# Optimization experiments

Hardware: AMD Instinct MI355X
Metric: run time of the kernel (lower is better)

Reference implementation:

```python
import jax, jax.numpy as jnp
import numpy as np

B, N, C, H = 2, 2048, 256, 16
D = C // H  # head_dim = 16


def _res_linear(x, W, b):
    # ResidualMLP with num_layers=-1 and in_dim==out_dim, input/output residual: x + Linear(x)
    return x + x @ W.T + b


def _split_heads(z):
    # [B, N, H*D] -> [B, H, N, D]
    return z.reshape(B, N, H, D).transpose(0, 2, 1, 3)


def setup_inputs() -> dict:
    key = jax.random.key(0)
    ks = jax.random.split(key, 10)
    def lin(k):
        return 0.02 * jax.random.normal(k, (C, C), dtype=jnp.float32)
    inp = {
        'x': jax.random.normal(ks[0], (B, N, C), dtype=jnp.float32),
        'attention_mask': jnp.ones((B, N), dtype=jnp.float32),
        'Wq1': lin(ks[1]), 'bq1': jnp.zeros((C,), jnp.float32),
        'Wq2': lin(ks[2]), 'bq2': jnp.zeros((C,), jnp.float32),
        'Wq3': lin(ks[3]), 'bq3': jnp.zeros((C,), jnp.float32),
        'Wk1': lin(ks[4]), 'bk1': jnp.zeros((C,), jnp.float32),
        'Wk2': lin(ks[5]), 'bk2': jnp.zeros((C,), jnp.float32),
        'Wk3': lin(ks[6]), 'bk3': jnp.zeros((C,), jnp.float32),
        'Wv': lin(ks[7]), 'bv': jnp.zeros((C,), jnp.float32),
        'Wo': lin(ks[8]), 'bo': jnp.zeros((C,), jnp.float32),
        'gamma': jnp.ones((C,), jnp.float32),
        'beta': jnp.zeros((C,), jnp.float32),
    }
    return inp


def reference(x, attention_mask, Wq1, bq1, Wq2, bq2, Wq3, bq3,
              Wk1, bk1, Wk2, bk2, Wk3, bk3, Wv, bv, Wo, bo, gamma, beta):
    # residual single-linear projections (ResidualMLP num_layers=-1)
    q1 = _split_heads(_res_linear(x, Wq1, bq1))
    q2 = _split_heads(_res_linear(x, Wq2, bq2))
    q3 = _split_heads(_res_linear(x, Wq3, bq3))
    k1 = _split_heads(_res_linear(x, Wk1, bk1))
    k2 = _split_heads(_res_linear(x, Wk2, bk2))
    k3 = _split_heads(_res_linear(x, Wk3, bk3))
    v = _split_heads(_res_linear(x, Wv, bv))
    # kernel = identity; norm_q = norm_k = False
    mask = attention_mask[:, None, :, None]  # [B,1,N,1]
    q1, q2, q3 = q1 * mask, q2 * mask, q3 * mask
    k1, k2, k3, v = k1 * mask, k2 * mask, k3 * mask, v * mask
    scale = jnp.asarray(N, jnp.float32) ** -0.25
    k1, k2, k3, v = k1 * scale, k2 * scale, k3 * scale, v * scale
    # rank-4 state: [B,H,D,D,D,D]
    state = jnp.einsum('bhni,bhnj,bhnk,bhnl->bhijkl', k1, v, k2, k3, optimize=True)
    # contract queries with state: [B,H,N,D]
    out = jnp.einsum('bhni,bhijkl,bhnk,bhnl->bhnj', q1, state, q2, q3, optimize=True)
    out = out.transpose(0, 2, 1, 3).reshape(B, N, C)  # merge heads
    # LayerNorm(channel_dim), eps=1e-5
    mu = jnp.mean(out, axis=-1, keepdims=True)
    var = jnp.mean(jnp.square(out - mu), axis=-1, keepdims=True)
    out = (out - mu) * jax.lax.rsqrt(var + 1e-5) * gamma + beta
    out = out @ Wo.T + bo
    return out
```

## Files before the change

kernel.cpp:

```cpp
#include <hip/hip_runtime.h>
#include <hip/hip_bf16.h>


typedef _Float16 f16;
typedef _Float16 f16x8 __attribute__((ext_vector_type(8)));
typedef _Float16 f16x4 __attribute__((ext_vector_type(4)));
typedef float    f32x16 __attribute__((ext_vector_type(16)));
typedef uint32_t u32x4 __attribute__((ext_vector_type(4)));

#define MFMA32(a, b, c) __builtin_amdgcn_mfma_f32_32x32x16_f16((a), (b), (c), 0, 0, 0)

constexpr size_t OFF_XH  = 0;
constexpr size_t OFF_WH  = 2097152;
constexpr size_t OFF_BSC = 3014656;
constexpr size_t OFF_GH  = 3021824;
constexpr size_t OFF_RSG = 3152896;
constexpr size_t OFF_B2  = 3153920;
constexpr size_t OFF_Y   = 3154944;
constexpr size_t OFF_KH  = 9446400;
constexpr size_t OFF_VT  = 15737856;
constexpr size_t OFF_OPP = 17835008;

struct W7 { const float* W[7]; const float* b[7]; };

__device__ __forceinline__ int toff(int row, int oct) {
    return row * 128 + (((oct) ^ (row & 7)) << 4);
}
__device__ __forceinline__ f16x8 ldfrag(const f16* base, int row, int oct) {
    return *(const f16x8*)((const char*)base + toff(row, oct));
}
__device__ __forceinline__ void stfrag(f16* base, int row, int oct, f16x8 v) {
    *(f16x8*)((char*)base + toff(row, oct)) = v;
}
__device__ __forceinline__ int drow(int reg, int l) {
    return (reg & 3) + ((reg >> 2) << 3) + ((l >> 5) << 2);
}
__device__ __forceinline__ void zero16(f32x16& v) {
#pragma unroll
    for (int i = 0; i < 16; ++i) v[i] = 0.f;
}
__device__ __forceinline__ uint32_t pkrtz(float a, float b) {
    auto h = __builtin_amdgcn_cvt_pkrtz(a, b);
    return __builtin_bit_cast(uint32_t, h);
}

__global__ __launch_bounds__(256) void k_prep(const float* __restrict__ x, W7 p,
                                              float scale,
                                              const float* __restrict__ Wo,
                                              const float* __restrict__ bo,
                                              const float* __restrict__ gamma,
                                              const float* __restrict__ beta,
                                              char* ws) {
    const int bid = blockIdx.x;
    if (bid < 2824) {
        f16* xh  = (f16*)(ws + OFF_XH);
        f16* Wh  = (f16*)(ws + OFF_WH);
        float* bsc = (float*)(ws + OFF_BSC);
        int idx = bid * 256 + threadIdx.x;
        if (idx < 262144) {
            float4 v = ((const float4*)x)[idx];
            f16x4 o; o[0] = (f16)v.x; o[1] = (f16)v.y; o[2] = (f16)v.z; o[3] = (f16)v.w;
            *(f16x4*)(xh + (size_t)idx * 4) = o;
        } else if (idx < 262144 + 458752) {
            int r = idx - 262144;
            int t = r >> 16, cc = r & 65535, c = cc >> 8, k = cc & 255;
            float v = p.W[t][cc] + (c == k ? 1.f : 0.f);
            if (t >= 3) v *= scale;
            Wh[r] = (f16)v;
        } else if (idx < 262144 + 458752 + 1792) {
            int r = idx - 262144 - 458752;
            int t = r >> 8;
            bsc[r] = p.b[t][r & 255] * (t >= 3 ? scale : 1.f);
        }
    } else {
        f16* Gh = (f16*)(ws + OFF_GH);
        float* rsg = (float*)(ws + OFF_RSG);
        float* B2  = (float*)(ws + OFF_B2);
        int c2 = bid - 2824, c = threadIdx.x;
        float wv = Wo[c2 * 256 + c];
        float g = gamma[c] * wv;
        float bb = beta[c] * wv;
        Gh[c2 * 256 + c] = (f16)g;
        __shared__ float sg[4], sb[4];
#pragma unroll
        for (int off = 32; off > 0; off >>= 1) { g += __shfl_down(g, off); bb += __shfl_down(bb, off); }
        if ((c & 63) == 0) { sg[c >> 6] = g; sb[c >> 6] = bb; }
        __syncthreads();
        if (c == 0) {
            rsg[c2] = sg[0] + sg[1] + sg[2] + sg[3];
            B2[c2]  = sb[0] + sb[1] + sb[2] + sb[3] + bo[c2];
        }
    }
}

__global__ __launch_bounds__(512) void k_lin7(const float* __restrict__ mask, char* ws) {
    const f16* xh = (const f16*)(ws + OFF_XH);
    const f16* Wh = (const f16*)(ws + OFF_WH);
    const float* bsc = (const float*)(ws + OFF_BSC);
    f16* Y  = (f16*)(ws + OFF_Y);
    f16* Kh = (f16*)(ws + OFF_KH);
    f16* Vt = (f16*)(ws + OFF_VT);

    const int ct = blockIdx.x;
    const int rt = blockIdx.y;
    const int t = ct >> 1, half = ct & 1;
    const int tid = threadIdx.x, l = tid & 63, w = tid >> 6;
    const int wr = w >> 1, wc = w & 1;

    __shared__ f16 Xl[128 * 64];
    __shared__ f16 Wl[128 * 64];

    f32x16 acc[2];
    zero16(acc[0]); zero16(acc[1]);

    const f16* Wt = Wh + (size_t)t * 65536;
    for (int kt = 0; kt < 4; ++kt) {
        __syncthreads();
#pragma unroll
        for (int e = 0; e < 2; ++e) {
            int g = tid + 512 * e;
            int row = g >> 3, oct = g & 7;
            f16x8 vx = *(const f16x8*)(xh + (size_t)(rt * 128 + row) * 256 + kt * 64 + oct * 8);
            stfrag(Xl, row, oct, vx);
            f16x8 vw = *(const f16x8*)(Wt + (size_t)(half * 128 + row) * 256 + kt * 64 + oct * 8);
            stfrag(Wl, row, oct, vw);
        }
        __syncthreads();
#pragma unroll
        for (int s = 0; s < 4; ++s) {
            int g = s * 2 + (l >> 5);
            f16x8 a0 = ldfrag(Xl, wr * 32 + (l & 31), g);
            f16x8 b0 = ldfrag(Wl, wc * 64 + (l & 31), g);
            f16x8 b1 = ldfrag(Wl, wc * 64 + 32 + (l & 31), g);
            acc[0] = MFMA32(a0, b0, acc[0]);
            acc[1] = MFMA32(a0, b1, acc[1]);
        }
    }

#pragma unroll
    for (int mc = 0; mc < 2; ++mc)
#pragma unroll
        for (int reg = 0; reg < 16; ++reg) {
            int n = rt * 128 + wr * 32 + drow(reg, l);
            int c = half * 128 + wc * 64 + mc * 32 + (l & 31);
            float v = (acc[mc][reg] + bsc[t * 256 + c]) * mask[n];
            f16 hv = (f16)v;
            if (t < 3) {
                Y[(size_t)t * 1048576 + (size_t)n * 256 + c] = hv;
            } else {
                int bb = n >> 11, m = n & 2047, h16 = c >> 4, d = c & 15;
                int bhx = bb * 16 + h16;
                if (t < 6) {
                    Kh[((size_t)(t - 3) * 32 + bhx) * 32768 + m * 16 + d] = hv;
                } else {
                    int m15 = m & 15;
                    int mp = (m & ~15) | (m15 & 3) | ((m15 & 4) << 1) | ((m15 & 8) >> 1);
                    Vt[(size_t)bhx * 32768 + (mp >> 3) * 128 + d * 8 + (mp & 7)] = hv;
                }
            }
        }
}

__global__ __launch_bounds__(256, 2) void k_attn(char* ws) {
    const f16* Y  = (const f16*)(ws + OFF_Y);
    const f16* Kh = (const f16*)(ws + OFF_KH);
    const f16* Vt = (const f16*)(ws + OFF_VT);
    f16* OPP = (f16*)(ws + OFF_OPP);

    const int lin = blockIdx.x + 8 * (blockIdx.y + 32 * blockIdx.z);
    const int work = (lin & 7) * 64 + (lin >> 3);
    const int nt = work & 7;
    const int bh = (work >> 3) & 31;
    const int ms = work >> 8;

    const int b = bh >> 4, hb = (bh & 15) * 16;
    const int tid = threadIdx.x, l = tid & 63, w = tid >> 6;
    const int lane31 = l & 31, lhi = l >> 5;
    const int n0 = nt * 256 + w * 64;
    const int jj = lane31 & 15;

    f16x8 qf[3][2];
#pragma unroll
    for (int t = 0; t < 3; ++t)
#pragma unroll
        for (int nn = 0; nn < 2; ++nn)
            qf[t][nn] = *(const f16x8*)(Y + (size_t)t * 1048576 +
                        ((size_t)(b * 2048 + n0 + nn * 32 + lane31)) * 256 + hb + lhi * 8);

    f32x16 accA[2], accB[2];
    zero16(accA[0]); zero16(accA[1]);
    zero16(accB[0]); zero16(accB[1]);
    f32x16 zzz; zero16(zzz);

    const f16* Kb0 = Kh + (size_t)bh * 32768 + (ms * 1024 + lane31) * 16 + lhi * 8;
    const f16* Kb1 = Kb0 + 1048576;
    const f16* Kb2 = Kb1 + 1048576;
    const f16* Vb  = Vt + (size_t)bh * 32768 + ms * 16384 + lhi * 128 + jj * 8;

    f16x8 kf0p[2], kf1p[2], kf2p[2], bv1p[2], bv2p[2];
#pragma unroll
    for (int s = 0; s < 2; ++s) {
        const int o = s * 512;
        kf0p[s] = *(const f16x8*)(Kb0 + o);
        kf1p[s] = *(const f16x8*)(Kb1 + o);
        kf2p[s] = *(const f16x8*)(Kb2 + o);
        bv1p[s] = *(const f16x8*)(Vb + o);
        bv2p[s] = *(const f16x8*)(Vb + o + 256);
    }

#pragma unroll 2
    for (int c = 0; c < 32; ++c) {
        const int slot = c & 1;
        f16x8 kf0 = kf0p[slot], kf1 = kf1p[slot], kf2 = kf2p[slot];
        f16x8 bv1 = bv1p[slot], bv2 = bv2p[slot];
        if (c < 30) {
            const int o = (c + 2) * 512;
            kf0p[slot] = *(const f16x8*)(Kb0 + o);
            kf1p[slot] = *(const f16x8*)(Kb1 + o);
            kf2p[slot] = *(const f16x8*)(Kb2 + o);
            bv1p[slot] = *(const f16x8*)(Vb + o);
            bv2p[slot] = *(const f16x8*)(Vb + o + 256);
        }
        __builtin_amdgcn_s_setprio(1);
#pragma unroll
        for (int nn = 0; nn < 2; ++nn) {
            f32x16 D1 = MFMA32(kf0, qf[0][nn], zzz);
            f32x16 D2 = MFMA32(kf1, qf[1][nn], zzz);
            f32x16 D3 = MFMA32(kf2, qf[2][nn], zzz);
            D1 *= D2;
            D1 *= D3;
            uint32_t p01 = pkrtz(D1[0], D1[1]),   p23 = pkrtz(D1[2], D1[3]);
            uint32_t p45 = pkrtz(D1[4], D1[5]),   p67 = pkrtz(D1[6], D1[7]);
            uint32_t p89 = pkrtz(D1[8], D1[9]),   pAB = pkrtz(D1[10], D1[11]);
            uint32_t pCD = pkrtz(D1[12], D1[13]), pEF = pkrtz(D1[14], D1[15]);
            u32x4 A1 = {p01, p23, p45, p67};
            u32x4 A2 = {p89, pAB, pCD, pEF};
            accA[nn] = MFMA32(__builtin_bit_cast(f16x8, A1), bv1, accA[nn]);
            accB[nn] = MFMA32(__builtin_bit_cast(f16x8, A2), bv2, accB[nn]);
        }
        __builtin_amdgcn_s_setprio(0);
    }

    if (lane31 < 16) {
        f16* outp = OPP + (size_t)ms * 1048576;
#pragma unroll
        for (int nn = 0; nn < 2; ++nn)
#pragma unroll
            for (int reg = 0; reg < 16; ++reg) {
                int n = n0 + nn * 32 + drow(reg, l);
                outp[((size_t)(b * 2048) + n) * 256 + hb + lane31] =
                    (f16)(accA[nn][reg] + accB[nn][reg]);
            }
    }
}

__global__ __launch_bounds__(256) void k_final(float* __restrict__ out, char* ws) {
    const f16* P0 = (const f16*)(ws + OFF_OPP);
    const f16* P1 = P0 + 1048576;
    const f16* Gh = (const f16*)(ws + OFF_GH);
    const float* rsg = (const float*)(ws + OFF_RSG);
    const float* B2 = (const float*)(ws + OFF_B2);

    const int ct = blockIdx.x;
    const int rt = blockIdx.y;
    const int tid = threadIdx.x, l = tid & 63, w = tid >> 6;
    const int wr = w >> 1, wc = w & 1;

    __shared__ f16 Xl[64 * 64];
    __shared__ f16 Wl[64 * 64];
    __shared__ float muL[64], rsL[64];

    float sum[2] = {0.f, 0.f}, sumsq[2] = {0.f, 0.f};

    f32x16 acc; zero16(acc);

    for (int kt = 0; kt < 4; ++kt) {
        __syncthreads();
#pragma unroll
        for (int e = 0; e < 2; ++e) {
            int g = tid + 256 * e;
            int row = g >> 3, oct = g & 7;
            size_t idx = (size_t)(rt * 64 + row) * 256 + kt * 64 + oct * 8;
            f16x8 va = *(const f16x8*)(P0 + idx);
            f16x8 vb = *(const f16x8*)(P1 + idx);
            f16x8 vx;
#pragma unroll
            for (int q = 0; q < 8; ++q) {
                float f = (float)va[q] + (float)vb[q];
                vx[q] = (f16)f;
                sum[e] += f; sumsq[e] += f * f;
            }
            stfrag(Xl, row, oct, vx);
            f16x8 vw = *(const f16x8*)(Gh + (size_t)(ct * 64 + row) * 256 + kt * 64 + oct * 8);
            stfrag(Wl, row, oct, vw);
        }
        __syncthreads();
#pragma unroll
        for (int s = 0; s < 4; ++s) {
            int g = s * 2 + (l >> 5);
            f16x8 a0 = ldfrag(Xl, wr * 32 + (l & 31), g);
            f16x8 b0 = ldfrag(Wl, wc * 32 + (l & 31), g);
            acc = MFMA32(a0, b0, acc);
        }
    }

#pragma unroll
    for (int e = 0; e < 2; ++e) {
#pragma unroll
        for (int off = 1; off < 8; off <<= 1) {
            sum[e] += __shfl_xor(sum[e], off);
            sumsq[e] += __shfl_xor(sumsq[e], off);
        }
    }
    if ((tid & 7) == 0) {
#pragma unroll
        for (int e = 0; e < 2; ++e) {
            int row = (tid >> 3) + 32 * e;
            float m = sum[e] * (1.f / 256.f);
            float var = sumsq[e] * (1.f / 256.f) - m * m;
            muL[row] = m;
            rsL[row] = rsqrtf(var + 1e-5f);
        }
    }
    __syncthreads();

#pragma unroll
    for (int reg = 0; reg < 16; ++reg) {
        int nloc = wr * 32 + drow(reg, l);
        int n = rt * 64 + nloc;
        int c2 = ct * 64 + wc * 32 + (l & 31);
        float v = rsL[nloc] * (acc[reg] - muL[nloc] * rsg[c2]) + B2[c2];
        out[(size_t)n * 256 + c2] = v;
    }
}

extern "C" void kernel_launch(void* const* d_in, const int* in_sizes, int n_in,
                              void* d_out, int out_size, void* d_ws, size_t ws_size,
                              hipStream_t stream) {
    (void)in_sizes; (void)n_in; (void)out_size; (void)ws_size;
    const float* x    = (const float*)d_in[0];
    const float* mask = (const float*)d_in[1];
    W7 p;
    for (int t = 0; t < 7; ++t) {
        p.W[t] = (const float*)d_in[2 + 2 * t];
        p.b[t] = (const float*)d_in[3 + 2 * t];
    }
    const float* Wo    = (const float*)d_in[16];
    const float* bo    = (const float*)d_in[17];
    const float* gamma = (const float*)d_in[18];
    const float* beta  = (const float*)d_in[19];
    char* ws = (char*)d_ws;

    const float scale = 0.14865088937534013f;

    k_prep <<<3080, 256, 0, stream>>>(x, p, scale, Wo, bo, gamma, beta, ws);
    k_lin7 <<<dim3(14, 32), 512, 0, stream>>>(mask, ws);
    k_attn <<<dim3(8, 32, 2), 256, 0, stream>>>(ws);
    k_final<<<dim3(4, 64), 256, 0, stream>>>((float*)d_out, ws);
}
```

Measured before the change: 57.56 us.

## Repartition attention kernel: more queries per wave, four-way key split

Each wave in k_attn now processes 128 queries (four 32-row MFMA tiles) instead of 64, so each loaded key/value fragment is reused across twice as many query tiles. The key dimension is split into four partial sums instead of two, keeping the grid size at 512 blocks. Prefetch depth drops from two stages to one, and the two accumulators per tile are merged into one, which serialises those MFMAs. k_final now reads and sums four partial outputs, adding extra memory traffic.

```diff
diff --git a/kernel.cpp b/kernel.cpp
--- a/kernel.cpp
+++ b/kernel.cpp
@@ -167,63 +167,55 @@
     const f16* Vt = (const f16*)(ws + OFF_VT);
     f16* OPP = (f16*)(ws + OFF_OPP);
 
-    const int lin = blockIdx.x + 8 * (blockIdx.y + 32 * blockIdx.z);
+    const int lin = blockIdx.x + 4 * (blockIdx.y + 32 * blockIdx.z);
     const int work = (lin & 7) * 64 + (lin >> 3);
-    const int nt = work & 7;
-    const int bh = (work >> 3) & 31;
-    const int ms = work >> 8;
+    const int nt = work & 3;
+    const int bh = (work >> 2) & 31;
+    const int ms = work >> 7;
 
     const int b = bh >> 4, hb = (bh & 15) * 16;
     const int tid = threadIdx.x, l = tid & 63, w = tid >> 6;
     const int lane31 = l & 31, lhi = l >> 5;
-    const int n0 = nt * 256 + w * 64;
+    const int n0 = nt * 512 + w * 128;
     const int jj = lane31 & 15;
 
-    f16x8 qf[3][2];
+    f16x8 qf[3][4];
 #pragma unroll
     for (int t = 0; t < 3; ++t)
 #pragma unroll
-        for (int nn = 0; nn < 2; ++nn)
+        for (int nn = 0; nn < 4; ++nn)
             qf[t][nn] = *(const f16x8*)(Y + (size_t)t * 1048576 +
                         ((size_t)(b * 2048 + n0 + nn * 32 + lane31)) * 256 + hb + lhi * 8);
 
-    f32x16 accA[2], accB[2];
-    zero16(accA[0]); zero16(accA[1]);
-    zero16(accB[0]); zero16(accB[1]);
+    f32x16 acc[4];
+#pragma unroll
+    for (int nn = 0; nn < 4; ++nn) zero16(acc[nn]);
     f32x16 zzz; zero16(zzz);
 
-    const f16* Kb0 = Kh + (size_t)bh * 32768 + (ms * 1024 + lane31) * 16 + lhi * 8;
+    const f16* Kb0 = Kh + (size_t)bh * 32768 + (ms * 512 + lane31) * 16 + lhi * 8;
     const f16* Kb1 = Kb0 + 1048576;
     const f16* Kb2 = Kb1 + 1048576;
-    const f16* Vb  = Vt + (size_t)bh * 32768 + ms * 16384 + lhi * 128 + jj * 8;
-
-    f16x8 kf0p[2], kf1p[2], kf2p[2], bv1p[2], bv2p[2];
-#pragma unroll
-    for (int s = 0; s < 2; ++s) {
-        const int o = s * 512;
-        kf0p[s] = *(const f16x8*)(Kb0 + o);
-        kf1p[s] = *(const f16x8*)(Kb1 + o);
-        kf2p[s] = *(const f16x8*)(Kb2 + o);
-        bv1p[s] = *(const f16x8*)(Vb + o);
-        bv2p[s] = *(const f16x8*)(Vb + o + 256);
-    }
-
-#pragma unroll 2
-    for (int c = 0; c < 32; ++c) {
-        const int slot = c & 1;
-        f16x8 kf0 = kf0p[slot], kf1 = kf1p[slot], kf2 = kf2p[slot];
-        f16x8 bv1 = bv1p[slot], bv2 = bv2p[slot];
-        if (c < 30) {
-            const int o = (c + 2) * 512;
-            kf0p[slot] = *(const f16x8*)(Kb0 + o);
-            kf1p[slot] = *(const f16x8*)(Kb1 + o);
-            kf2p[slot] = *(const f16x8*)(Kb2 + o);
-            bv1p[slot] = *(const f16x8*)(Vb + o);
-            bv2p[slot] = *(const f16x8*)(Vb + o + 256);
+    const f16* Vb  = Vt + (size_t)bh * 32768 + ms * 8192 + lhi * 128 + jj * 8;
+
+    f16x8 kf0n = *(const f16x8*)(Kb0);
+    f16x8 kf1n = *(const f16x8*)(Kb1);
+    f16x8 kf2n = *(const f16x8*)(Kb2);
+    f16x8 bv1n = *(const f16x8*)(Vb);
+    f16x8 bv2n = *(const f16x8*)(Vb + 256);
+
+    for (int c = 0; c < 16; ++c) {
+        f16x8 kf0 = kf0n, kf1 = kf1n, kf2 = kf2n, bv1 = bv1n, bv2 = bv2n;
+        if (c < 15) {
+            const int o = (c + 1) * 512;
+            kf0n = *(const f16x8*)(Kb0 + o);
+            kf1n = *(const f16x8*)(Kb1 + o);
+            kf2n = *(const f16x8*)(Kb2 + o);
+            bv1n = *(const f16x8*)(Vb + o);
+            bv2n = *(const f16x8*)(Vb + o + 256);
         }
         __builtin_amdgcn_s_setprio(1);
 #pragma unroll
-        for (int nn = 0; nn < 2; ++nn) {
+        for (int nn = 0; nn < 4; ++nn) {
             f32x16 D1 = MFMA32(kf0, qf[0][nn], zzz);
             f32x16 D2 = MFMA32(kf1, qf[1][nn], zzz);
             f32x16 D3 = MFMA32(kf2, qf[2][nn], zzz);
@@ -235,8 +227,8 @@
             uint32_t pCD = pkrtz(D1[12], D1[13]), pEF = pkrtz(D1[14], D1[15]);
             u32x4 A1 = {p01, p23, p45, p67};
             u32x4 A2 = {p89, pAB, pCD, pEF};
-            accA[nn] = MFMA32(__builtin_bit_cast(f16x8, A1), bv1, accA[nn]);
-            accB[nn] = MFMA32(__builtin_bit_cast(f16x8, A2), bv2, accB[nn]);
+            acc[nn] = MFMA32(__builtin_bit_cast(f16x8, A1), bv1, acc[nn]);
+            acc[nn] = MFMA32(__builtin_bit_cast(f16x8, A2), bv2, acc[nn]);
         }
         __builtin_amdgcn_s_setprio(0);
     }
@@ -244,12 +236,11 @@
     if (lane31 < 16) {
         f16* outp = OPP + (size_t)ms * 1048576;
 #pragma unroll
-        for (int nn = 0; nn < 2; ++nn)
+        for (int nn = 0; nn < 4; ++nn)
 #pragma unroll
             for (int reg = 0; reg < 16; ++reg) {
                 int n = n0 + nn * 32 + drow(reg, l);
-                outp[((size_t)(b * 2048) + n) * 256 + hb + lane31] =
-                    (f16)(accA[nn][reg] + accB[nn][reg]);
+                outp[((size_t)(b * 2048) + n) * 256 + hb + lane31] = (f16)acc[nn][reg];
             }
     }
 }
@@ -257,6 +248,8 @@
 __global__ __launch_bounds__(256) void k_final(float* __restrict__ out, char* ws) {
     const f16* P0 = (const f16*)(ws + OFF_OPP);
     const f16* P1 = P0 + 1048576;
+    const f16* P2 = P1 + 1048576;
+    const f16* P3 = P2 + 1048576;
     const f16* Gh = (const f16*)(ws + OFF_GH);
     const float* rsg = (const float*)(ws + OFF_RSG);
     const float* B2 = (const float*)(ws + OFF_B2);
@@ -283,10 +276,12 @@
             size_t idx = (size_t)(rt * 64 + row) * 256 + kt * 64 + oct * 8;
             f16x8 va = *(const f16x8*)(P0 + idx);
             f16x8 vb = *(const f16x8*)(P1 + idx);
+            f16x8 vc = *(const f16x8*)(P2 + idx);
+            f16x8 vd = *(const f16x8*)(P3 + idx);
             f16x8 vx;
 #pragma unroll
             for (int q = 0; q < 8; ++q) {
-                float f = (float)va[q] + (float)vb[q];
+                float f = ((float)va[q] + (float)vb[q]) + ((float)vc[q] + (float)vd[q]);
                 vx[q] = (f16)f;
                 sum[e] += f; sumsq[e] += f * f;
             }
@@ -355,6 +350,6 @@
 
     k_prep <<<3080, 256, 0, stream>>>(x, p, scale, Wo, bo, gamma, beta, ws);
     k_lin7 <<<dim3(14, 32), 512, 0, stream>>>(mask, ws);
-    k_attn <<<dim3(8, 32, 2), 256, 0, stream>>>(ws);
+    k_attn <<<dim3(4, 32, 4), 256, 0, stream>>>(ws);
     k_final<<<dim3(4, 64), 256, 0, stream>>>((float*)d_out, ws);
 }
```

Measured after the change: 59.88 us. 1.04x slower.
